# Optimization experiments

Hardware: AMD Instinct MI355X
Metric: run time of the kernel (lower is better)

The kernel has to match this reference:

```python
import jax, jax.numpy as jnp
import numpy as np

B, T, D, M = 2048, 512, 8, 2  # groups, timesteps, state_rank, n_measures


def setup_inputs() -> dict:
    key = jax.random.key(0)
    ks = jax.random.split(key, 7)
    inp = jax.random.normal(ks[0], (B, T, M), dtype=jnp.float32)
    mean0 = 0.1 * jax.random.normal(ks[1], (B, D), dtype=jnp.float32)
    A = 0.1 * jax.random.normal(ks[2], (B, D, D), dtype=jnp.float32)
    cov0 = A @ jnp.swapaxes(A, -1, -2) + jnp.eye(D, dtype=jnp.float32)  # PSD initial cov
    F = 0.95 * jnp.eye(D, dtype=jnp.float32) + 0.01 * jax.random.normal(ks[3], (D, D), dtype=jnp.float32)
    H = jax.random.normal(ks[4], (M, D), dtype=jnp.float32)
    Aq = 0.1 * jax.random.normal(ks[5], (D, D), dtype=jnp.float32)
    Q = Aq @ Aq.T + 0.1 * jnp.eye(D, dtype=jnp.float32)
    Ar = 0.1 * jax.random.normal(ks[6], (M, M), dtype=jnp.float32)
    R = Ar @ Ar.T + 0.1 * jnp.eye(M, dtype=jnp.float32)
    return dict(input=inp, mean0=mean0, cov0=cov0, F=F, H=H, Q=Q, R=R)


def _kf_scan(input, mean0, cov0, F, H, Q, R):
    """n_step=1 Kalman recurrence: at t emit the 1-step-ahead prediction made
    from data up to t-1 (so output[0] is the initial state), matching
    ScriptKalmanFilter.forward with n_step=1."""

    def step(carry, x_t):
        mean, cov = carry  # [B,D], [B,D,D]
        # --- update ---
        HP = jnp.einsum('md,bde->bme', H, cov)                 # H P : [B,M,D]
        S = jnp.einsum('bme,ne->bmn', HP, H) + R               # innovation cov [B,M,M]
        Kt = jnp.linalg.solve(S, HP)                           # K^T = S^{-1} H P : [B,M,D]
        resid = x_t - jnp.einsum('md,bd->bm', H, mean)         # [B,M]
        mean_u = mean + jnp.einsum('bmd,bm->bd', Kt, resid)
        cov_u = cov - jnp.einsum('bmd,bme->bde', Kt, HP)       # (I-KH)P
        # --- predict ---
        mean_p = jnp.einsum('de,be->bd', F, mean_u)
        cov_p = jnp.einsum('de,bef,gf->bdg', F, cov_u, F) + Q  # F P F^T + Q
        return (mean_p, cov_p), (mean_p, cov_p)

    xs = jnp.swapaxes(input, 0, 1)  # [T,B,M]
    _, (means_s, covs_s) = jax.lax.scan(step, (mean0, cov0), xs)
    # output at step t is the state BEFORE consuming x_t (1-step-ahead)
    means = jnp.concatenate([mean0[None], means_s[:-1]], axis=0)  # [T,B,D]
    covs = jnp.concatenate([cov0[None], covs_s[:-1]], axis=0)     # [T,B,D,D]
    return jnp.swapaxes(means, 0, 1), jnp.swapaxes(covs, 0, 1)


def reference(input, mean0, cov0, F, H, Q, R):
    means, covs = _kf_scan(input, mean0, cov0, F, H, Q, R)
    b, t, m = input.shape
    Rs = jnp.broadcast_to(R, (b, t, m, m))      # stacked per-time R (static design)
    Hs = jnp.broadcast_to(H, (b, t, m, H.shape[-1]))
    return means, covs, Rs, Hs
```

## Files before the change

kernel.cpp:

```cpp
#include <hip/hip_runtime.h>

typedef float v2 __attribute__((ext_vector_type(2)));
typedef float v4 __attribute__((ext_vector_type(4)));

#define B_TOT 2048
#define T_STEPS 512

#define OFF_COVS 8388608
#define OFF_RS   75497472
#define OFF_HS   79691776

static __device__ __forceinline__ v2 sp(float s) { v2 r; r.x = s; r.y = s; return r; }

__launch_bounds__(64, 1)
__global__ void kf_kernel(const float* __restrict__ input,
                          const float* __restrict__ mean0,
                          const float* __restrict__ cov0,
                          const float* __restrict__ Fm,
                          const float* __restrict__ Hm,
                          const float* __restrict__ Qm,
                          const float* __restrict__ Rm,
                          float* __restrict__ out)
{
    __shared__ float xs[8 * 1024];
    __shared__ float hps[8 * 28];
    __shared__ float ws[8 * 84];
    __shared__ float mean_s[8 * 12];

    const int lane = threadIdx.x;
    const int g = lane >> 3;
    const int j = lane & 7;
    const int b0 = blockIdx.x * 8;
    const int b = b0 + g;

    {
        const v4* src = (const v4*)(input + (size_t)b0 * 1024);
        v4* dst = (v4*)xs;
        #pragma unroll
        for (int i = 0; i < 32; ++i)
            dst[i * 64 + lane] = src[i * 64 + lane];
    }

    v2 Fcol2[8][4];
    #pragma unroll
    for (int f = 0; f < 8; ++f)
        #pragma unroll
        for (int d2 = 0; d2 < 4; ++d2) {
            v2 t; t.x = Fm[(2 * d2) * 8 + f]; t.y = Fm[(2 * d2 + 1) * 8 + f];
            Fcol2[f][d2] = t;
        }
    v2 Frowj[4];
    #pragma unroll
    for (int d2 = 0; d2 < 4; ++d2) {
        v2 t; t.x = Fm[j * 8 + 2 * d2]; t.y = Fm[j * 8 + 2 * d2 + 1];
        Frowj[d2] = t;
    }
    v2 Hrow2[2][4];
    #pragma unroll
    for (int m = 0; m < 2; ++m)
        #pragma unroll
        for (int d2 = 0; d2 < 4; ++d2) {
            v2 t; t.x = Hm[m * 8 + 2 * d2]; t.y = Hm[m * 8 + 2 * d2 + 1];
            Hrow2[m][d2] = t;
        }
    v2 HFrow2[2][4];
    #pragma unroll
    for (int m = 0; m < 2; ++m)
        #pragma unroll
        for (int d2 = 0; d2 < 4; ++d2) {
            float a = 0.f, c = 0.f;
            #pragma unroll
            for (int k = 0; k < 8; ++k) {
                a += Hm[m * 8 + k] * Fm[k * 8 + 2 * d2];
                c += Hm[m * 8 + k] * Fm[k * 8 + 2 * d2 + 1];
            }
            v2 t; t.x = a; t.y = c; HFrow2[m][d2] = t;
        }
    v2 Qrow2[4];
    #pragma unroll
    for (int e2 = 0; e2 < 4; ++e2) {
        v2 t; t.x = Qm[j * 8 + 2 * e2]; t.y = Qm[j * 8 + 2 * e2 + 1];
        Qrow2[e2] = t;
    }
    const float r00 = Rm[0], r01 = Rm[1], r10 = Rm[2], r11 = Rm[3];
    const float Rval = (j == 0) ? r00 : (j == 1) ? r01 : (j == 2) ? r10 : r11;
    v2 Hflat; Hflat.x = Hm[2 * j]; Hflat.y = Hm[2 * j + 1];

    v2 P2[4];
    {
        const v4* c4 = (const v4*)(cov0 + (size_t)b * 64 + j * 8);
        v4 a = c4[0], bb = c4[1];
        P2[0].x = a.x;  P2[0].y = a.y;  P2[1].x = a.z;  P2[1].y = a.w;
        P2[2].x = bb.x; P2[2].y = bb.y; P2[3].x = bb.z; P2[3].y = bb.w;
    }
    float mean_j = mean0[(size_t)b * 8 + j];

    float hm0, hm1;
    mean_s[g * 12 + j] = mean_j;
    {
        const v4* ms = (const v4*)(mean_s + g * 12);
        v4 a = ms[0], bb = ms[1];
        v2 mu[4];
        mu[0].x = a.x;  mu[0].y = a.y;  mu[1].x = a.z;  mu[1].y = a.w;
        mu[2].x = bb.x; mu[2].y = bb.y; mu[3].x = bb.z; mu[3].y = bb.w;
        v2 t0 = {0.f, 0.f}, t1 = {0.f, 0.f};
        #pragma unroll
        for (int d2 = 0; d2 < 4; ++d2) { t0 += Hrow2[0][d2] * mu[d2]; t1 += Hrow2[1][d2] * mu[d2]; }
        hm0 = t0.x + t0.y; hm1 = t1.x + t1.y;
    }

    float* means_p = out + (size_t)b * T_STEPS * 8 + j;
    float* covs_p  = out + OFF_COVS + (size_t)b * T_STEPS * 64 + j * 8;
    float* Rs_p    = out + OFF_RS + (size_t)b * T_STEPS * 4 + j;
    float* Hs_p    = out + OFF_HS + (size_t)b * T_STEPS * 16 + 2 * j;
    const v2* xv   = (const v2*)(xs + g * 1024);

    v2 xcur = xv[0];

    for (int t = 0; t < T_STEPS; ++t) {
        v2 a0 = {0.f, 0.f}, a1 = {0.f, 0.f};
        #pragma unroll
        for (int d2 = 0; d2 < 4; ++d2) { a0 += Hrow2[0][d2] * P2[d2]; a1 += Hrow2[1][d2] * P2[d2]; }
        const float hp0 = a0.x + a0.y;
        const float hp1 = a1.x + a1.y;
        hps[g * 28 + j]      = hp0;
        hps[g * 28 + 10 + j] = hp1;

        v2 W2[4] = {{0.f,0.f},{0.f,0.f},{0.f,0.f},{0.f,0.f}};
        #pragma unroll
        for (int f = 0; f < 8; ++f) {
            const float pf = (f & 1) ? P2[f >> 1].y : P2[f >> 1].x;
            const v2 c = sp(pf);
            #pragma unroll
            for (int d2 = 0; d2 < 4; ++d2) W2[d2] += Fcol2[f][d2] * c;
        }
        #pragma unroll
        for (int d = 0; d < 8; ++d) {
            const float wd = (d & 1) ? W2[d >> 1].y : W2[d >> 1].x;
            ws[g * 84 + d * 10 + j] = wd;
        }

        means_p[0] = mean_j;
        {
            v4 cva, cvb;
            cva.x = P2[0].x; cva.y = P2[0].y; cva.z = P2[1].x; cva.w = P2[1].y;
            cvb.x = P2[2].x; cvb.y = P2[2].y; cvb.z = P2[3].x; cvb.w = P2[3].y;
            ((v4*)covs_p)[0] = cva;
            ((v4*)covs_p)[1] = cvb;
        }
        if (j < 4) Rs_p[0] = Rval;
        *((v2*)Hs_p) = Hflat;
        means_p += 8; covs_p += 64; Rs_p += 4; Hs_p += 16;

        const v2 xnext = xv[(t + 1) & (T_STEPS - 1)];

        v2 hpa0[4], hpa1[4];
        {
            const v2* p0 = (const v2*)(hps + g * 28);
            const v2* p1 = (const v2*)(hps + g * 28 + 10);
            #pragma unroll
            for (int f2 = 0; f2 < 4; ++f2) { hpa0[f2] = p0[f2]; hpa1[f2] = p1[f2]; }
        }

        v2 s00v = {0.f, 0.f}, s01v = {0.f, 0.f}, s11v = {0.f, 0.f};
        #pragma unroll
        for (int f2 = 0; f2 < 4; ++f2) {
            s00v += hpa0[f2] * Hrow2[0][f2];
            s01v += hpa0[f2] * Hrow2[1][f2];
            s11v += hpa1[f2] * Hrow2[1][f2];
        }
        const float s00 = s00v.x + s00v.y + r00;
        const float s01 = s01v.x + s01v.y + r01;
        const float s11 = s11v.x + s11v.y + r11;
        const float det = s00 * s11 - s01 * s01;
        const float idet = __builtin_amdgcn_rcpf(det);
        const float i00 = s11 * idet, i01 = -s01 * idet, i11 = s00 * idet;

        const float kt0 = i00 * hp0 + i01 * hp1;
        const float kt1 = i01 * hp0 + i11 * hp1;
        const float rs0 = xcur.x - hm0;
        const float rs1 = xcur.y - hm1;
        const float mean_u = mean_j + kt0 * rs0 + kt1 * rs1;
        mean_s[g * 12 + j] = mean_u;

        v2 dd0 = {0.f, 0.f}, dd1 = {0.f, 0.f};
        #pragma unroll
        for (int f2 = 0; f2 < 4; ++f2) { dd0 += Frowj[f2] * hpa0[f2]; dd1 += Frowj[f2] * hpa1[f2]; }
        const float d0 = dd0.x + dd0.y;
        const float d1 = dd1.x + dd1.y;
        const float c0 = i00 * d0 + i01 * d1;
        const float c1 = i01 * d0 + i11 * d1;
        const v2 c0v = sp(c0), c1v = sp(c1);
        v2 z[4];
        #pragma unroll
        for (int f2 = 0; f2 < 4; ++f2) z[f2] = c0v * hpa0[f2] + c1v * hpa1[f2];

        v2 Wr[4];
        {
            const v2* wp = (const v2*)(ws + g * 84 + j * 10);
            #pragma unroll
            for (int f2 = 0; f2 < 4; ++f2) Wr[f2] = wp[f2];
        }
        v2 mu2[4];
        {
            const v4* ms = (const v4*)(mean_s + g * 12);
            v4 a = ms[0], bb = ms[1];
            mu2[0].x = a.x;  mu2[0].y = a.y;  mu2[1].x = a.z;  mu2[1].y = a.w;
            mu2[2].x = bb.x; mu2[2].y = bb.y; mu2[3].x = bb.z; mu2[3].y = bb.w;
        }

        v2 Wt[4];
        #pragma unroll
        for (int f2 = 0; f2 < 4; ++f2) Wt[f2] = Wr[f2] - z[f2];
        v2 Pn[4] = {Qrow2[0], Qrow2[1], Qrow2[2], Qrow2[3]};
        #pragma unroll
        for (int f = 0; f < 8; ++f) {
            const float wtf = (f & 1) ? Wt[f >> 1].y : Wt[f >> 1].x;
            const v2 c = sp(wtf);
            #pragma unroll
            for (int e2 = 0; e2 < 4; ++e2) Pn[e2] += Fcol2[f][e2] * c;
        }
        P2[0] = Pn[0]; P2[1] = Pn[1]; P2[2] = Pn[2]; P2[3] = Pn[3];

        v2 t0 = {0.f, 0.f}, t1 = {0.f, 0.f}, t2 = {0.f, 0.f};
        #pragma unroll
        for (int d2 = 0; d2 < 4; ++d2) {
            t0 += Frowj[d2] * mu2[d2];
            t1 += HFrow2[0][d2] * mu2[d2];
            t2 += HFrow2[1][d2] * mu2[d2];
        }
        mean_j = t0.x + t0.y;
        hm0 = t1.x + t1.y;
        hm1 = t2.x + t2.y;
        xcur = xnext;
    }
}

extern "C" void kernel_launch(void* const* d_in, const int* in_sizes, int n_in,
                              void* d_out, int out_size, void* d_ws, size_t ws_size,
                              hipStream_t stream) {
    const float* input = (const float*)d_in[0];
    const float* mean0 = (const float*)d_in[1];
    const float* cov0  = (const float*)d_in[2];
    const float* F     = (const float*)d_in[3];
    const float* H     = (const float*)d_in[4];
    const float* Q     = (const float*)d_in[5];
    const float* R     = (const float*)d_in[6];
    float* out = (float*)d_out;

    hipLaunchKernelGGL(kf_kernel, dim3(B_TOT / 8), dim3(64), 0, stream,
                       input, mean0, cov0, F, H, Q, R, out);
}
```

Measured before the change: 588.1 us.

## Replicate mean state per lane and merge shared-memory exchange buffers

Every lane of an 8-lane group now holds the full mean vector and computes the mean update and F·mean prediction redundantly. This removes the second shared-memory round trip per timestep for the mean. The HP and W exchange buffers are merged into one compact per-group region read with wide vector loads, and means are written as two v4 stores from lane 0 only. The cost is extra redundant ALU work per lane and a serialized lane-0 store of the means.

```diff
diff --git a/kernel.cpp b/kernel.cpp
--- a/kernel.cpp
+++ b/kernel.cpp
@@ -9,6 +9,8 @@
 #define OFF_COVS 8388608
 #define OFF_RS   75497472
 #define OFF_HS   79691776
+
+#define CSTR 104
 
 static __device__ __forceinline__ v2 sp(float s) { v2 r; r.x = s; r.y = s; return r; }
 
@@ -23,9 +25,7 @@
                           float* __restrict__ out)
 {
     __shared__ float xs[8 * 1024];
-    __shared__ float hps[8 * 28];
-    __shared__ float ws[8 * 84];
-    __shared__ float mean_s[8 * 12];
+    __shared__ float comm[8 * CSTR];
 
     const int lane = threadIdx.x;
     const int g = lane >> 3;
@@ -62,19 +62,6 @@
         for (int d2 = 0; d2 < 4; ++d2) {
             v2 t; t.x = Hm[m * 8 + 2 * d2]; t.y = Hm[m * 8 + 2 * d2 + 1];
             Hrow2[m][d2] = t;
-        }
-    v2 HFrow2[2][4];
-    #pragma unroll
-    for (int m = 0; m < 2; ++m)
-        #pragma unroll
-        for (int d2 = 0; d2 < 4; ++d2) {
-            float a = 0.f, c = 0.f;
-            #pragma unroll
-            for (int k = 0; k < 8; ++k) {
-                a += Hm[m * 8 + k] * Fm[k * 8 + 2 * d2];
-                c += Hm[m * 8 + k] * Fm[k * 8 + 2 * d2 + 1];
-            }
-            v2 t; t.x = a; t.y = c; HFrow2[m][d2] = t;
         }
     v2 Qrow2[4];
     #pragma unroll
@@ -93,27 +80,20 @@
         P2[0].x = a.x;  P2[0].y = a.y;  P2[1].x = a.z;  P2[1].y = a.w;
         P2[2].x = bb.x; P2[2].y = bb.y; P2[3].x = bb.z; P2[3].y = bb.w;
     }
-    float mean_j = mean0[(size_t)b * 8 + j];
-
-    float hm0, hm1;
-    mean_s[g * 12 + j] = mean_j;
+    v2 mn[4];
     {
-        const v4* ms = (const v4*)(mean_s + g * 12);
-        v4 a = ms[0], bb = ms[1];
-        v2 mu[4];
-        mu[0].x = a.x;  mu[0].y = a.y;  mu[1].x = a.z;  mu[1].y = a.w;
-        mu[2].x = bb.x; mu[2].y = bb.y; mu[3].x = bb.z; mu[3].y = bb.w;
-        v2 t0 = {0.f, 0.f}, t1 = {0.f, 0.f};
-        #pragma unroll
-        for (int d2 = 0; d2 < 4; ++d2) { t0 += Hrow2[0][d2] * mu[d2]; t1 += Hrow2[1][d2] * mu[d2]; }
-        hm0 = t0.x + t0.y; hm1 = t1.x + t1.y;
-    }
-
-    float* means_p = out + (size_t)b * T_STEPS * 8 + j;
+        const v4* m4 = (const v4*)(mean0 + (size_t)b * 8);
+        v4 a = m4[0], bb = m4[1];
+        mn[0].x = a.x;  mn[0].y = a.y;  mn[1].x = a.z;  mn[1].y = a.w;
+        mn[2].x = bb.x; mn[2].y = bb.y; mn[3].x = bb.z; mn[3].y = bb.w;
+    }
+
+    float* means_p = out + (size_t)b * T_STEPS * 8;
     float* covs_p  = out + OFF_COVS + (size_t)b * T_STEPS * 64 + j * 8;
     float* Rs_p    = out + OFF_RS + (size_t)b * T_STEPS * 4 + j;
     float* Hs_p    = out + OFF_HS + (size_t)b * T_STEPS * 16 + 2 * j;
     const v2* xv   = (const v2*)(xs + g * 1024);
+    float* cm      = comm + g * CSTR;
 
     v2 xcur = xv[0];
 
@@ -123,8 +103,6 @@
         for (int d2 = 0; d2 < 4; ++d2) { a0 += Hrow2[0][d2] * P2[d2]; a1 += Hrow2[1][d2] * P2[d2]; }
         const float hp0 = a0.x + a0.y;
         const float hp1 = a1.x + a1.y;
-        hps[g * 28 + j]      = hp0;
-        hps[g * 28 + 10 + j] = hp1;
 
         v2 W2[4] = {{0.f,0.f},{0.f,0.f},{0.f,0.f},{0.f,0.f}};
         #pragma unroll
@@ -134,13 +112,22 @@
             #pragma unroll
             for (int d2 = 0; d2 < 4; ++d2) W2[d2] += Fcol2[f][d2] * c;
         }
+
         #pragma unroll
         for (int d = 0; d < 8; ++d) {
             const float wd = (d & 1) ? W2[d >> 1].y : W2[d >> 1].x;
-            ws[g * 84 + d * 10 + j] = wd;
-        }
-
-        means_p[0] = mean_j;
+            cm[d * 8 + j] = wd;
+        }
+        cm[64 + j] = hp0;
+        cm[72 + j] = hp1;
+
+        if (j == 0) {
+            v4 mva, mvb;
+            mva.x = mn[0].x; mva.y = mn[0].y; mva.z = mn[1].x; mva.w = mn[1].y;
+            mvb.x = mn[2].x; mvb.y = mn[2].y; mvb.z = mn[3].x; mvb.w = mn[3].y;
+            ((v4*)means_p)[0] = mva;
+            ((v4*)means_p)[1] = mvb;
+        }
         {
             v4 cva, cvb;
             cva.x = P2[0].x; cva.y = P2[0].y; cva.z = P2[1].x; cva.w = P2[1].y;
@@ -154,12 +141,24 @@
 
         const v2 xnext = xv[(t + 1) & (T_STEPS - 1)];
 
-        v2 hpa0[4], hpa1[4];
-        {
-            const v2* p0 = (const v2*)(hps + g * 28);
-            const v2* p1 = (const v2*)(hps + g * 28 + 10);
-            #pragma unroll
-            for (int f2 = 0; f2 < 4; ++f2) { hpa0[f2] = p0[f2]; hpa1[f2] = p1[f2]; }
+        v2 t0 = {0.f, 0.f}, t1 = {0.f, 0.f};
+        #pragma unroll
+        for (int d2 = 0; d2 < 4; ++d2) { t0 += Hrow2[0][d2] * mn[d2]; t1 += Hrow2[1][d2] * mn[d2]; }
+        const float hm0 = t0.x + t0.y;
+        const float hm1 = t1.x + t1.y;
+
+        v2 hpa0[4], hpa1[4], Wr[4];
+        {
+            const v4* hp4 = (const v4*)(cm + 64);
+            v4 ha = hp4[0], hb = hp4[1], hc = hp4[2], hd = hp4[3];
+            hpa0[0].x = ha.x; hpa0[0].y = ha.y; hpa0[1].x = ha.z; hpa0[1].y = ha.w;
+            hpa0[2].x = hb.x; hpa0[2].y = hb.y; hpa0[3].x = hb.z; hpa0[3].y = hb.w;
+            hpa1[0].x = hc.x; hpa1[0].y = hc.y; hpa1[1].x = hc.z; hpa1[1].y = hc.w;
+            hpa1[2].x = hd.x; hpa1[2].y = hd.y; hpa1[3].x = hd.z; hpa1[3].y = hd.w;
+            const v4* w4 = (const v4*)(cm + j * 8);
+            v4 wa = w4[0], wb = w4[1];
+            Wr[0].x = wa.x; Wr[0].y = wa.y; Wr[1].x = wa.z; Wr[1].y = wa.w;
+            Wr[2].x = wb.x; Wr[2].y = wb.y; Wr[3].x = wb.z; Wr[3].y = wb.w;
         }
 
         v2 s00v = {0.f, 0.f}, s01v = {0.f, 0.f}, s11v = {0.f, 0.f};
@@ -176,12 +175,27 @@
         const float idet = __builtin_amdgcn_rcpf(det);
         const float i00 = s11 * idet, i01 = -s01 * idet, i11 = s00 * idet;
 
-        const float kt0 = i00 * hp0 + i01 * hp1;
-        const float kt1 = i01 * hp0 + i11 * hp1;
         const float rs0 = xcur.x - hm0;
         const float rs1 = xcur.y - hm1;
-        const float mean_u = mean_j + kt0 * rs0 + kt1 * rs1;
-        mean_s[g * 12 + j] = mean_u;
+        const float aa0 = i00 * rs0 + i01 * rs1;
+        const float aa1 = i01 * rs0 + i11 * rs1;
+        v2 mu[4];
+        {
+            const v2 av0 = sp(aa0), av1 = sp(aa1);
+            #pragma unroll
+            for (int d2 = 0; d2 < 4; ++d2) mu[d2] = mn[d2] + av0 * hpa0[d2] + av1 * hpa1[d2];
+        }
+        {
+            v2 nm[4] = {{0.f,0.f},{0.f,0.f},{0.f,0.f},{0.f,0.f}};
+            #pragma unroll
+            for (int e = 0; e < 8; ++e) {
+                const float me = (e & 1) ? mu[e >> 1].y : mu[e >> 1].x;
+                const v2 c = sp(me);
+                #pragma unroll
+                for (int d2 = 0; d2 < 4; ++d2) nm[d2] += Fcol2[e][d2] * c;
+            }
+            mn[0] = nm[0]; mn[1] = nm[1]; mn[2] = nm[2]; mn[3] = nm[3];
+        }
 
         v2 dd0 = {0.f, 0.f}, dd1 = {0.f, 0.f};
         #pragma unroll
@@ -190,48 +204,24 @@
         const float d1 = dd1.x + dd1.y;
         const float c0 = i00 * d0 + i01 * d1;
         const float c1 = i01 * d0 + i11 * d1;
-        const v2 c0v = sp(c0), c1v = sp(c1);
-        v2 z[4];
-        #pragma unroll
-        for (int f2 = 0; f2 < 4; ++f2) z[f2] = c0v * hpa0[f2] + c1v * hpa1[f2];
-
-        v2 Wr[4];
-        {
-            const v2* wp = (const v2*)(ws + g * 84 + j * 10);
-            #pragma unroll
-            for (int f2 = 0; f2 < 4; ++f2) Wr[f2] = wp[f2];
-        }
-        v2 mu2[4];
-        {
-            const v4* ms = (const v4*)(mean_s + g * 12);
-            v4 a = ms[0], bb = ms[1];
-            mu2[0].x = a.x;  mu2[0].y = a.y;  mu2[1].x = a.z;  mu2[1].y = a.w;
-            mu2[2].x = bb.x; mu2[2].y = bb.y; mu2[3].x = bb.z; mu2[3].y = bb.w;
-        }
-
         v2 Wt[4];
-        #pragma unroll
-        for (int f2 = 0; f2 < 4; ++f2) Wt[f2] = Wr[f2] - z[f2];
-        v2 Pn[4] = {Qrow2[0], Qrow2[1], Qrow2[2], Qrow2[3]};
-        #pragma unroll
-        for (int f = 0; f < 8; ++f) {
-            const float wtf = (f & 1) ? Wt[f >> 1].y : Wt[f >> 1].x;
-            const v2 c = sp(wtf);
-            #pragma unroll
-            for (int e2 = 0; e2 < 4; ++e2) Pn[e2] += Fcol2[f][e2] * c;
-        }
-        P2[0] = Pn[0]; P2[1] = Pn[1]; P2[2] = Pn[2]; P2[3] = Pn[3];
-
-        v2 t0 = {0.f, 0.f}, t1 = {0.f, 0.f}, t2 = {0.f, 0.f};
-        #pragma unroll
-        for (int d2 = 0; d2 < 4; ++d2) {
-            t0 += Frowj[d2] * mu2[d2];
-            t1 += HFrow2[0][d2] * mu2[d2];
-            t2 += HFrow2[1][d2] * mu2[d2];
-        }
-        mean_j = t0.x + t0.y;
-        hm0 = t1.x + t1.y;
-        hm1 = t2.x + t2.y;
+        {
+            const v2 c0v = sp(c0), c1v = sp(c1);
+            #pragma unroll
+            for (int f2 = 0; f2 < 4; ++f2) Wt[f2] = Wr[f2] - c0v * hpa0[f2] - c1v * hpa1[f2];
+        }
+        {
+            v2 Pn[4] = {Qrow2[0], Qrow2[1], Qrow2[2], Qrow2[3]};
+            #pragma unroll
+            for (int f = 0; f < 8; ++f) {
+                const float wtf = (f & 1) ? Wt[f >> 1].y : Wt[f >> 1].x;
+                const v2 c = sp(wtf);
+                #pragma unroll
+                for (int e2 = 0; e2 < 4; ++e2) Pn[e2] += Fcol2[f][e2] * c;
+            }
+            P2[0] = Pn[0]; P2[1] = Pn[1]; P2[2] = Pn[2]; P2[3] = Pn[3];
+        }
+
         xcur = xnext;
     }
 }
```

New measurement: 592.8 us. About the same (+0.8%).
